# Kernel optimization log

Hardware: AMD Instinct MI355X
Metric: run time of the kernel (lower is better)

Reference implementation:

```python
import jax, jax.numpy as jnp
import numpy as np
import math

B, C, H, W = 8, 512, 32, 32
NUM_HEADS = 8          # channels // num_head_channels = 512 // 64
NUM_GROUPS = 32        # GroupNorm32
EPS = 1e-5


def setup_inputs() -> dict:
    key = jax.random.key(0)
    k1, k2, k3, k4, k5 = jax.random.split(key, 5)
    x = jax.random.normal(k1, (B, C, H, W), dtype=jnp.float32)
    # GroupNorm affine params (torch init: ones/zeros)
    norm_scale = jnp.ones((C,), dtype=jnp.float32)
    norm_bias = jnp.zeros((C,), dtype=jnp.float32)
    # 1x1 Conv1d weights: qkv maps C -> 3C, proj maps C -> C
    qkv_w = jax.random.normal(k2, (3 * C, C), dtype=jnp.float32) * 0.02
    qkv_b = jax.random.normal(k3, (3 * C,), dtype=jnp.float32) * 0.02
    # NOTE: original zero-inits proj_out; we use small random weights so the
    # block computes non-trivial math (same op structure, same FLOPs).
    proj_w = jax.random.normal(k4, (C, C), dtype=jnp.float32) * 0.02
    proj_b = jax.random.normal(k5, (C,), dtype=jnp.float32) * 0.02
    return {"x": x, "norm_scale": norm_scale, "norm_bias": norm_bias,
            "qkv_w": qkv_w, "qkv_b": qkv_b, "proj_w": proj_w, "proj_b": proj_b}


def _attention_block(x, norm_scale, norm_bias, qkv_w, qkv_b, proj_w, proj_b):
    b, c, h, w = x.shape
    t = h * w
    xf = x.reshape(b, c, t)
    # GroupNorm32: fp32 compute, 32 groups, biased variance, eps=1e-5
    g = xf.astype(jnp.float32).reshape(b, NUM_GROUPS, c // NUM_GROUPS, t)
    mean = g.mean(axis=(2, 3), keepdims=True)
    var = g.var(axis=(2, 3), keepdims=True)
    gn = ((g - mean) * jax.lax.rsqrt(var + EPS)).reshape(b, c, t)
    gn = (gn * norm_scale[None, :, None] + norm_bias[None, :, None]).astype(xf.dtype)
    # 1x1 conv == channel matmul: [B,C,T] -> [B,3C,T]
    qkv = jnp.einsum('oc,bct->bot', qkv_w, gn) + qkv_b[None, :, None]
    # Legacy head layout: [B, H*3*ch, T] -> [B*H, 3*ch, T]
    ch = c // NUM_HEADS
    qkv = qkv.reshape(b * NUM_HEADS, 3 * ch, t)
    q, k, v = jnp.split(qkv, 3, axis=1)          # each [B*H, ch, T]
    scale = 1.0 / math.sqrt(math.sqrt(ch))
    weight = jnp.einsum('bct,bcs->bts', q * scale, k * scale)  # [B*H, T, T]
    weight = jax.nn.softmax(weight.astype(jnp.float32), axis=-1).astype(qkv.dtype)
    a = jnp.einsum('bts,bcs->bct', weight, v).reshape(b, c, t)
    out = jnp.einsum('oc,bct->bot', proj_w, a) + proj_b[None, :, None]
    return (xf + out).reshape(b, c, h, w)


def reference(x, norm_scale, norm_bias, qkv_w, qkv_b, proj_w, proj_b):
    return _attention_block(x, norm_scale, norm_bias, qkv_w, qkv_b, proj_w, proj_b)
```

## Files before the change

kernel.cpp:

```cpp
#include <hip/hip_runtime.h>
#include <math.h>

#define B_   8
#define C_   512
#define T_   1024
#define G_   32
#define CPG  16
#define NH   8
#define OC3  1536
#define EPS  1e-5f

#define QSCALE 0.18033688011112042f
#define C_OFF  11.541560327111708f

typedef __bf16 bf16;
typedef __bf16 bf16x4 __attribute__((ext_vector_type(4)));
typedef __bf16 bf16x8 __attribute__((ext_vector_type(8)));
typedef float  f32x4  __attribute__((ext_vector_type(4)));

#define MFMA16(a, b, c) __builtin_amdgcn_mfma_f32_16x16x32_bf16((a), (b), (c), 0, 0, 0)

__device__ __forceinline__ float fexp2(float x) {
#if defined(__has_builtin)
#if __has_builtin(__builtin_amdgcn_exp2f)
    return __builtin_amdgcn_exp2f(x);
#else
    return __expf(x * 0.6931471805599453f);
#endif
#else
    return __expf(x * 0.6931471805599453f);
#endif
}

__global__ __launch_bounds__(256) void cvt_w(const float* __restrict__ w,
                                             bf16* __restrict__ wb)
{
    int i = blockIdx.x * 256 + threadIdx.x;
    float4 v = ((const float4*)w)[i];
    bf16x4 o;
    o[0] = (bf16)v.x; o[1] = (bf16)v.y; o[2] = (bf16)v.z; o[3] = (bf16)v.w;
    *(bf16x4*)(wb + (size_t)i * 4) = o;
}

__global__ __launch_bounds__(256) void gn_kernel(const float* __restrict__ x,
                                                 const float* __restrict__ scale,
                                                 const float* __restrict__ bias,
                                                 bf16* __restrict__ gnT)
{
    const int blk = blockIdx.x;
    const int b = blk >> 5, g = blk & 31;
    const size_t base = (size_t)blk * (CPG * T_);
    const float4* xin = (const float4*)(x + base);
    const int tid = threadIdx.x;

    float s = 0.f, ss = 0.f;
    float4 vals[16];
#pragma unroll
    for (int i = 0; i < 16; ++i) {
        float4 v = xin[tid + i * 256];
        vals[i] = v;
        s  += v.x + v.y + v.z + v.w;
        ss += v.x * v.x + v.y * v.y + v.z * v.z + v.w * v.w;
    }

    __shared__ float rs[256], rss[256];
    rs[tid] = s; rss[tid] = ss;
    __syncthreads();
    for (int off = 128; off > 0; off >>= 1) {
        if (tid < off) { rs[tid] += rs[tid + off]; rss[tid] += rss[tid + off]; }
        __syncthreads();
    }
    const float invN = 1.f / (float)(CPG * T_);
    const float mean = rs[0] * invN;
    const float var  = rss[0] * invN - mean * mean;
    const float inv  = rsqrtf(var + EPS);

    const int c0 = g * CPG;
    float sc[16], bi[16];
#pragma unroll
    for (int i = 0; i < 16; ++i) {
        float s_ = scale[c0 + i] * inv;
        sc[i] = s_;
        bi[i] = bias[c0 + i] - mean * s_;
    }
    bf16* ob = gnT + (size_t)b * (T_ * C_) + c0;
#pragma unroll
    for (int tt = 0; tt < 4; ++tt) {
        bf16x8 lo, hi;
#pragma unroll
        for (int i = 0; i < 8; ++i) {
            float v0 = (tt == 0) ? vals[i].x : (tt == 1) ? vals[i].y
                     : (tt == 2) ? vals[i].z : vals[i].w;
            float v1 = (tt == 0) ? vals[i + 8].x : (tt == 1) ? vals[i + 8].y
                     : (tt == 2) ? vals[i + 8].z : vals[i + 8].w;
            lo[i] = (bf16)(v0 * sc[i] + bi[i]);
            hi[i] = (bf16)(v1 * sc[i + 8] + bi[i + 8]);
        }
        bf16* p = ob + (size_t)(4 * tid + tt) * C_;
        *(bf16x8*)p       = lo;
        *(bf16x8*)(p + 8) = hi;
    }
}

__global__ __launch_bounds__(256) void qkv_gemm(const bf16* __restrict__ gnT,
                                                const bf16* __restrict__ Wb,
                                                const float* __restrict__ qkv_b,
                                                bf16* __restrict__ qkvT)
{
    const int b   = blockIdx.z;
    const int seg = blockIdx.y;
    const int o0  = seg * 64;
    const int t0  = blockIdx.x * 64;
    const int tid = threadIdx.x;
    const int lane = tid & 63;
    const int wv   = tid >> 6;
    const int tg = wv >> 1, og = wv & 1;
    const int lq = lane & 15, lg = lane >> 4;

    __shared__ __align__(16) bf16 Ag[64][72];
    __shared__ __align__(16) bf16 Bg[64][72];

    const bf16* gA = gnT + (size_t)b * (T_ * C_) + (size_t)t0 * C_;
    const bf16* gB = Wb + (size_t)o0 * C_;

    f32x4 acc[2][2];
#pragma unroll
    for (int i = 0; i < 2; ++i)
#pragma unroll
        for (int j = 0; j < 2; ++j) { acc[i][j][0]=0.f; acc[i][j][1]=0.f; acc[i][j][2]=0.f; acc[i][j][3]=0.f; }

    for (int k0 = 0; k0 < C_; k0 += 64) {
#pragma unroll
        for (int it = 0; it < 2; ++it) {
            int c = tid + it * 256;
            int r = c >> 3, cp = c & 7;
            *(bf16x8*)&Ag[r][cp * 8] = *(const bf16x8*)(gA + (size_t)r * C_ + k0 + cp * 8);
            *(bf16x8*)&Bg[r][cp * 8] = *(const bf16x8*)(gB + (size_t)r * C_ + k0 + cp * 8);
        }
        __syncthreads();
        bf16x8 af[2][2], bfr[2][2];
#pragma unroll
        for (int mf = 0; mf < 2; ++mf)
#pragma unroll
            for (int kb = 0; kb < 2; ++kb) {
                af[mf][kb]  = *(const bf16x8*)&Ag[tg * 32 + mf * 16 + lq][kb * 32 + lg * 8];
                bfr[mf][kb] = *(const bf16x8*)&Bg[og * 32 + mf * 16 + lq][kb * 32 + lg * 8];
            }
#pragma unroll
        for (int mf = 0; mf < 2; ++mf)
#pragma unroll
            for (int nf = 0; nf < 2; ++nf) {
                acc[mf][nf] = MFMA16(af[mf][0], bfr[nf][0], acc[mf][nf]);
                acc[mf][nf] = MFMA16(af[mf][1], bfr[nf][1], acc[mf][nf]);
            }
        __syncthreads();
    }

    const int which = seg % 3;
    bf16* outb = qkvT + (size_t)(b * 24 + seg) * (T_ * 64);
    if (which != 2) {
        const float osc = (which == 0) ? QSCALE : 1.0f;
#pragma unroll
        for (int nf = 0; nf < 2; ++nf) {
            int ch = og * 32 + nf * 16 + lq;
            float bias = qkv_b[o0 + ch];
#pragma unroll
            for (int mf = 0; mf < 2; ++mf) {
                int tb = t0 + tg * 32 + mf * 16 + lg * 4;
#pragma unroll
                for (int r = 0; r < 4; ++r)
                    outb[(size_t)(tb + r) * 64 + ch] = (bf16)((acc[mf][nf][r] + bias) * osc);
            }
        }
    } else {
#pragma unroll
        for (int nf = 0; nf < 2; ++nf) {
            int ch = og * 32 + nf * 16 + lq;
            float bias = qkv_b[o0 + ch];
#pragma unroll
            for (int mf = 0; mf < 2; ++mf) {
                int tb = t0 + tg * 32 + mf * 16 + lg * 4;
                bf16x4 pb;
#pragma unroll
                for (int r = 0; r < 4; ++r) pb[r] = (bf16)(acc[mf][nf][r] + bias);
                *(bf16x4*)(outb + (size_t)ch * T_ + tb) = pb;
            }
        }
    }
}

__global__ __launch_bounds__(256) void attn_kernel(const bf16* __restrict__ qkvT,
                                                   bf16* __restrict__ aT)
{
    const int id = blockIdx.x;
    const int bh = id & 63;
    const int tile = id >> 6;
    const int tid = threadIdx.x;
    const int lane = tid & 63;
    const int w  = tid >> 6;
    const int lq = lane & 15;
    const int lg = lane >> 4;
    const int q0 = tile * 128 + w * 32;

    const bf16* qb = qkvT + (size_t)(bh * 3 + 0) * (T_ * 64);
    const bf16* kb = qkvT + (size_t)(bh * 3 + 1) * (T_ * 64);
    const bf16* vb = qkvT + (size_t)(bh * 3 + 2) * (T_ * 64);

    __shared__ __align__(16) bf16 ks[64][72];
    __shared__ __align__(16) bf16 vs[64][72];
    __shared__ __align__(16) bf16 ps[4][32][72];

    bf16x8 qf[2][2];
#pragma unroll
    for (int qg = 0; qg < 2; ++qg)
#pragma unroll
        for (int kh = 0; kh < 2; ++kh)
            qf[qg][kh] = *(const bf16x8*)(qb + (size_t)(q0 + qg * 16 + lq) * 64 + kh * 32 + lg * 8);

    f32x4 oacc[2][4];
#pragma unroll
    for (int qg = 0; qg < 2; ++qg)
#pragma unroll
        for (int og = 0; og < 4; ++og) { oacc[qg][og][0]=0.f; oacc[qg][og][1]=0.f; oacc[qg][og][2]=0.f; oacc[qg][og][3]=0.f; }
    float lloc[2] = {0.f, 0.f};

    const int sr = tid >> 3, scp = tid & 7;
    bf16x8 kreg[2], vreg[2];
#pragma unroll
    for (int it = 0; it < 2; ++it) {
        kreg[it] = *(const bf16x8*)(kb + (size_t)(sr + it * 32) * 64 + scp * 8);
        vreg[it] = *(const bf16x8*)(vb + (size_t)(sr + it * 32) * T_ + scp * 8);
    }

    for (int s0 = 0; s0 < T_; s0 += 64) {
        __syncthreads();
#pragma unroll
        for (int it = 0; it < 2; ++it) {
            *(bf16x8*)&ks[sr + it * 32][scp * 8] = kreg[it];
            *(bf16x8*)&vs[sr + it * 32][scp * 8] = vreg[it];
        }
        __syncthreads();
        if (s0 + 64 < T_) {
            int sn = s0 + 64;
#pragma unroll
            for (int it = 0; it < 2; ++it) {
                kreg[it] = *(const bf16x8*)(kb + (size_t)(sn + sr + it * 32) * 64 + scp * 8);
                vreg[it] = *(const bf16x8*)(vb + (size_t)(sr + it * 32) * T_ + sn + scp * 8);
            }
        }

        f32x4 st[2][4];
        f32x4 cinit; cinit[0] = -C_OFF; cinit[1] = -C_OFF; cinit[2] = -C_OFF; cinit[3] = -C_OFF;
#pragma unroll
        for (int g = 0; g < 4; ++g) {
            bf16x8 kf0 = *(const bf16x8*)&ks[g * 16 + lq][lg * 8];
            bf16x8 kf1 = *(const bf16x8*)&ks[g * 16 + lq][32 + lg * 8];
#pragma unroll
            for (int qg = 0; qg < 2; ++qg) {
                st[qg][g] = MFMA16(kf0, qf[qg][0], cinit);
                st[qg][g] = MFMA16(kf1, qf[qg][1], st[qg][g]);
            }
        }
#pragma unroll
        for (int qg = 0; qg < 2; ++qg) {
            float ll = 0.f;
#pragma unroll
            for (int g = 0; g < 4; ++g) {
                bf16x4 pb;
#pragma unroll
                for (int r = 0; r < 4; ++r) {
                    float p = fexp2(st[qg][g][r]);
                    ll += p;
                    pb[r] = (bf16)p;
                }
                *(bf16x4*)&ps[w][qg * 16 + lq][g * 16 + lg * 4] = pb;
            }
            lloc[qg] += ll;
        }
        bf16x8 pa[2][2];
#pragma unroll
        for (int qg = 0; qg < 2; ++qg)
#pragma unroll
            for (int kh = 0; kh < 2; ++kh)
                pa[qg][kh] = *(const bf16x8*)&ps[w][qg * 16 + lq][kh * 32 + lg * 8];
#pragma unroll
        for (int og = 0; og < 4; ++og) {
            bf16x8 vf0 = *(const bf16x8*)&vs[og * 16 + lq][lg * 8];
            bf16x8 vf1 = *(const bf16x8*)&vs[og * 16 + lq][32 + lg * 8];
#pragma unroll
            for (int qg = 0; qg < 2; ++qg) {
                oacc[qg][og] = MFMA16(pa[qg][0], vf0, oacc[qg][og]);
                oacc[qg][og] = MFMA16(pa[qg][1], vf1, oacc[qg][og]);
            }
        }
    }

    const int b = bh >> 3, h = bh & 7;
#pragma unroll
    for (int qg = 0; qg < 2; ++qg) {
        float l = lloc[qg];
        l += __shfl_xor(l, 16);
        l += __shfl_xor(l, 32);
        float linv = 1.f / l;
        float li[4];
#pragma unroll
        for (int r = 0; r < 4; ++r) li[r] = __shfl(linv, lg * 4 + r);
        bf16* ob = aT + ((size_t)b * T_ + q0 + qg * 16 + lg * 4) * C_ + h * 64 + lq;
#pragma unroll
        for (int og = 0; og < 4; ++og)
#pragma unroll
            for (int r = 0; r < 4; ++r)
                ob[(size_t)r * C_ + og * 16] = (bf16)(oacc[qg][og][r] * li[r]);
    }
}

__global__ __launch_bounds__(256) void proj_gemm(const bf16* __restrict__ aT,
                                                 const bf16* __restrict__ PWb,
                                                 const float* __restrict__ proj_b,
                                                 const float* __restrict__ x,
                                                 float* __restrict__ out)
{
    const int b   = blockIdx.z;
    const int o0  = blockIdx.y * 64;
    const int t0  = blockIdx.x * 64;
    const int tid = threadIdx.x;
    const int lane = tid & 63;
    const int wv   = tid >> 6;
    const int tg = wv >> 1, og = wv & 1;
    const int lq = lane & 15, lg = lane >> 4;

    __shared__ __align__(16) bf16 Ag[64][72];
    __shared__ __align__(16) bf16 Bg[64][72];

    const bf16* gA = aT + (size_t)b * (T_ * C_) + (size_t)t0 * C_;
    const bf16* gB = PWb + (size_t)o0 * C_;

    f32x4 acc[2][2];
#pragma unroll
    for (int i = 0; i < 2; ++i)
#pragma unroll
        for (int j = 0; j < 2; ++j) { acc[i][j][0]=0.f; acc[i][j][1]=0.f; acc[i][j][2]=0.f; acc[i][j][3]=0.f; }

    for (int k0 = 0; k0 < C_; k0 += 64) {
#pragma unroll
        for (int it = 0; it < 2; ++it) {
            int c = tid + it * 256;
            int r = c >> 3, cp = c & 7;
            *(bf16x8*)&Ag[r][cp * 8] = *(const bf16x8*)(gA + (size_t)r * C_ + k0 + cp * 8);
            *(bf16x8*)&Bg[r][cp * 8] = *(const bf16x8*)(gB + (size_t)r * C_ + k0 + cp * 8);
        }
        __syncthreads();
        bf16x8 af[2][2], bfr[2][2];
#pragma unroll
        for (int mf = 0; mf < 2; ++mf)
#pragma unroll
            for (int kb = 0; kb < 2; ++kb) {
                af[mf][kb]  = *(const bf16x8*)&Ag[tg * 32 + mf * 16 + lq][kb * 32 + lg * 8];
                bfr[mf][kb] = *(const bf16x8*)&Bg[og * 32 + mf * 16 + lq][kb * 32 + lg * 8];
            }
#pragma unroll
        for (int mf = 0; mf < 2; ++mf)
#pragma unroll
            for (int nf = 0; nf < 2; ++nf) {
                acc[mf][nf] = MFMA16(af[mf][0], bfr[nf][0], acc[mf][nf]);
                acc[mf][nf] = MFMA16(af[mf][1], bfr[nf][1], acc[mf][nf]);
            }
        __syncthreads();
    }

#pragma unroll
    for (int nf = 0; nf < 2; ++nf) {
        int o = o0 + og * 32 + nf * 16 + lq;
        float bias = proj_b[o];
#pragma unroll
        for (int mf = 0; mf < 2; ++mf) {
            int tb = t0 + tg * 32 + mf * 16 + lg * 4;
            size_t idx = ((size_t)b * C_ + o) * T_ + tb;
            float4 xr = *(const float4*)(x + idx);
            float4 rv;
            rv.x = acc[mf][nf][0] + bias + xr.x;
            rv.y = acc[mf][nf][1] + bias + xr.y;
            rv.z = acc[mf][nf][2] + bias + xr.z;
            rv.w = acc[mf][nf][3] + bias + xr.w;
            *(float4*)(out + idx) = rv;
        }
    }
}

extern "C" void kernel_launch(void* const* d_in, const int* in_sizes, int n_in,
                              void* d_out, int out_size, void* d_ws, size_t ws_size,
                              hipStream_t stream)
{
    (void)in_sizes; (void)n_in; (void)out_size; (void)ws_size;
    const float* x      = (const float*)d_in[0];
    const float* nscale = (const float*)d_in[1];
    const float* nbias  = (const float*)d_in[2];
    const float* qkv_w  = (const float*)d_in[3];
    const float* qkv_b  = (const float*)d_in[4];
    const float* proj_w = (const float*)d_in[5];
    const float* proj_b = (const float*)d_in[6];
    float* out = (float*)d_out;

    char* wsb = (char*)d_ws;
    bf16*  gnT  = (bf16*) (wsb);
    bf16*  Wb   = (bf16*) (wsb + (size_t)(8  << 20));
    bf16*  PWb  = Wb + (size_t)OC3 * C_;
    bf16*  qkvT = (bf16*) (wsb + (size_t)(12 << 20));
    bf16*  aT   = (bf16*) (wsb + (size_t)(36 << 20));

    cvt_w<<<768, 256, 0, stream>>>(qkv_w, Wb);
    cvt_w<<<256, 256, 0, stream>>>(proj_w, PWb);
    gn_kernel<<<B_ * G_, 256, 0, stream>>>(x, nscale, nbias, gnT);
    qkv_gemm<<<dim3(T_ / 64, OC3 / 64, B_), 256, 0, stream>>>(gnT, Wb, qkv_b, qkvT);
    attn_kernel<<<512, 256, 0, stream>>>(qkvT, aT);
    proj_gemm<<<dim3(T_ / 64, C_ / 64, B_), 256, 0, stream>>>(aT, PWb, proj_b, x, out);
}
```

Before: 86.92 us.

## Merge QKV and proj GEMMs into 128x128-tile kernel with register prefetch

```diff
diff --git a/kernel.cpp b/kernel.cpp
--- a/kernel.cpp
+++ b/kernel.cpp
@@ -102,88 +102,122 @@
     }
 }
 
-__global__ __launch_bounds__(256) void qkv_gemm(const bf16* __restrict__ gnT,
-                                                const bf16* __restrict__ Wb,
-                                                const float* __restrict__ qkv_b,
-                                                bf16* __restrict__ qkvT)
+template <int MODE>
+__global__ __launch_bounds__(256) void mm128(const bf16* __restrict__ Arows,
+                                             const bf16* __restrict__ Wt,
+                                             const float* __restrict__ bias,
+                                             const float* __restrict__ x,
+                                             void* __restrict__ outp)
 {
     const int b   = blockIdx.z;
-    const int seg = blockIdx.y;
-    const int o0  = seg * 64;
-    const int t0  = blockIdx.x * 64;
+    const int o0  = blockIdx.y * 128;
+    const int t0  = blockIdx.x * 128;
     const int tid = threadIdx.x;
     const int lane = tid & 63;
-    const int wv   = tid >> 6;
-    const int tg = wv >> 1, og = wv & 1;
+    const int w  = tid >> 6;
+    const int wr = w >> 1, wc = w & 1;
     const int lq = lane & 15, lg = lane >> 4;
 
-    __shared__ __align__(16) bf16 Ag[64][72];
-    __shared__ __align__(16) bf16 Bg[64][72];
-
-    const bf16* gA = gnT + (size_t)b * (T_ * C_) + (size_t)t0 * C_;
-    const bf16* gB = Wb + (size_t)o0 * C_;
-
-    f32x4 acc[2][2];
-#pragma unroll
-    for (int i = 0; i < 2; ++i)
-#pragma unroll
-        for (int j = 0; j < 2; ++j) { acc[i][j][0]=0.f; acc[i][j][1]=0.f; acc[i][j][2]=0.f; acc[i][j][3]=0.f; }
+    __shared__ __align__(16) bf16 Ag[128][72];
+    __shared__ __align__(16) bf16 Bg[128][72];
+
+    const bf16* gA = Arows + (size_t)b * (T_ * C_) + (size_t)t0 * C_;
+    const bf16* gB = Wt + (size_t)o0 * C_;
+
+    f32x4 acc[4][4];
+#pragma unroll
+    for (int i = 0; i < 4; ++i)
+#pragma unroll
+        for (int j = 0; j < 4; ++j) { acc[i][j][0]=0.f; acc[i][j][1]=0.f; acc[i][j][2]=0.f; acc[i][j][3]=0.f; }
+
+    bf16x8 areg[4], breg[4];
+#pragma unroll
+    for (int it = 0; it < 4; ++it) {
+        int chunk = it * 256 + tid, row = chunk >> 3, cp = chunk & 7;
+        areg[it] = *(const bf16x8*)(gA + (size_t)row * C_ + cp * 8);
+        breg[it] = *(const bf16x8*)(gB + (size_t)row * C_ + cp * 8);
+    }
 
     for (int k0 = 0; k0 < C_; k0 += 64) {
-#pragma unroll
-        for (int it = 0; it < 2; ++it) {
-            int c = tid + it * 256;
-            int r = c >> 3, cp = c & 7;
-            *(bf16x8*)&Ag[r][cp * 8] = *(const bf16x8*)(gA + (size_t)r * C_ + k0 + cp * 8);
-            *(bf16x8*)&Bg[r][cp * 8] = *(const bf16x8*)(gB + (size_t)r * C_ + k0 + cp * 8);
-        }
-        __syncthreads();
-        bf16x8 af[2][2], bfr[2][2];
-#pragma unroll
-        for (int mf = 0; mf < 2; ++mf)
-#pragma unroll
-            for (int kb = 0; kb < 2; ++kb) {
-                af[mf][kb]  = *(const bf16x8*)&Ag[tg * 32 + mf * 16 + lq][kb * 32 + lg * 8];
-                bfr[mf][kb] = *(const bf16x8*)&Bg[og * 32 + mf * 16 + lq][kb * 32 + lg * 8];
-            }
-#pragma unroll
-        for (int mf = 0; mf < 2; ++mf)
-#pragma unroll
-            for (int nf = 0; nf < 2; ++nf) {
-                acc[mf][nf] = MFMA16(af[mf][0], bfr[nf][0], acc[mf][nf]);
-                acc[mf][nf] = MFMA16(af[mf][1], bfr[nf][1], acc[mf][nf]);
-            }
-        __syncthreads();
-    }
-
-    const int which = seg % 3;
-    bf16* outb = qkvT + (size_t)(b * 24 + seg) * (T_ * 64);
-    if (which != 2) {
-        const float osc = (which == 0) ? QSCALE : 1.0f;
-#pragma unroll
-        for (int nf = 0; nf < 2; ++nf) {
-            int ch = og * 32 + nf * 16 + lq;
-            float bias = qkv_b[o0 + ch];
-#pragma unroll
-            for (int mf = 0; mf < 2; ++mf) {
-                int tb = t0 + tg * 32 + mf * 16 + lg * 4;
-#pragma unroll
-                for (int r = 0; r < 4; ++r)
-                    outb[(size_t)(tb + r) * 64 + ch] = (bf16)((acc[mf][nf][r] + bias) * osc);
+        __syncthreads();
+#pragma unroll
+        for (int it = 0; it < 4; ++it) {
+            int chunk = it * 256 + tid, row = chunk >> 3, cp = chunk & 7;
+            *(bf16x8*)&Ag[row][cp * 8] = areg[it];
+            *(bf16x8*)&Bg[row][cp * 8] = breg[it];
+        }
+        __syncthreads();
+        if (k0 + 64 < C_) {
+#pragma unroll
+            for (int it = 0; it < 4; ++it) {
+                int chunk = it * 256 + tid, row = chunk >> 3, cp = chunk & 7;
+                areg[it] = *(const bf16x8*)(gA + (size_t)row * C_ + k0 + 64 + cp * 8);
+                breg[it] = *(const bf16x8*)(gB + (size_t)row * C_ + k0 + 64 + cp * 8);
+            }
+        }
+#pragma unroll
+        for (int kb = 0; kb < 2; ++kb) {
+            bf16x8 af[4], bfr[4];
+#pragma unroll
+            for (int i = 0; i < 4; ++i) {
+                af[i]  = *(const bf16x8*)&Ag[wr * 64 + i * 16 + lq][kb * 32 + lg * 8];
+                bfr[i] = *(const bf16x8*)&Bg[wc * 64 + i * 16 + lq][kb * 32 + lg * 8];
+            }
+#pragma unroll
+            for (int mf = 0; mf < 4; ++mf)
+#pragma unroll
+                for (int nf = 0; nf < 4; ++nf)
+                    acc[mf][nf] = MFMA16(af[mf], bfr[nf], acc[mf][nf]);
+        }
+    }
+
+    if (MODE == 0) {
+        bf16* qkvT = (bf16*)outp;
+#pragma unroll
+        for (int nf = 0; nf < 4; ++nf) {
+            int chg = o0 + wc * 64 + nf * 16 + lq;
+            int seg = chg >> 6;
+            int which = seg % 3;
+            int chs = chg & 63;
+            float bv = bias[chg];
+            bf16* outb = qkvT + (size_t)(b * 24 + seg) * (T_ * 64);
+            if (which != 2) {
+                float osc = (which == 0) ? QSCALE : 1.0f;
+#pragma unroll
+                for (int mf = 0; mf < 4; ++mf) {
+                    int tb = t0 + wr * 64 + mf * 16 + lg * 4;
+#pragma unroll
+                    for (int r = 0; r < 4; ++r)
+                        outb[(size_t)(tb + r) * 64 + chs] = (bf16)((acc[mf][nf][r] + bv) * osc);
+                }
+            } else {
+#pragma unroll
+                for (int mf = 0; mf < 4; ++mf) {
+                    int tb = t0 + wr * 64 + mf * 16 + lg * 4;
+                    bf16x4 pb;
+#pragma unroll
+                    for (int r = 0; r < 4; ++r) pb[r] = (bf16)(acc[mf][nf][r] + bv);
+                    *(bf16x4*)(outb + (size_t)chs * T_ + tb) = pb;
+                }
             }
         }
     } else {
-#pragma unroll
-        for (int nf = 0; nf < 2; ++nf) {
-            int ch = og * 32 + nf * 16 + lq;
-            float bias = qkv_b[o0 + ch];
-#pragma unroll
-            for (int mf = 0; mf < 2; ++mf) {
-                int tb = t0 + tg * 32 + mf * 16 + lg * 4;
-                bf16x4 pb;
-#pragma unroll
-                for (int r = 0; r < 4; ++r) pb[r] = (bf16)(acc[mf][nf][r] + bias);
-                *(bf16x4*)(outb + (size_t)ch * T_ + tb) = pb;
+        float* out = (float*)outp;
+#pragma unroll
+        for (int nf = 0; nf < 4; ++nf) {
+            int o = o0 + wc * 64 + nf * 16 + lq;
+            float bv = bias[o];
+#pragma unroll
+            for (int mf = 0; mf < 4; ++mf) {
+                int tb = t0 + wr * 64 + mf * 16 + lg * 4;
+                size_t idx = ((size_t)b * C_ + o) * T_ + tb;
+                float4 xr = *(const float4*)(x + idx);
+                float4 rv;
+                rv.x = acc[mf][nf][0] + bv + xr.x;
+                rv.y = acc[mf][nf][1] + bv + xr.y;
+                rv.z = acc[mf][nf][2] + bv + xr.z;
+                rv.w = acc[mf][nf][3] + bv + xr.w;
+                *(float4*)(out + idx) = rv;
             }
         }
     }
@@ -314,79 +348,6 @@
     }
 }
 
-__global__ __launch_bounds__(256) void proj_gemm(const bf16* __restrict__ aT,
-                                                 const bf16* __restrict__ PWb,
-                                                 const float* __restrict__ proj_b,
-                                                 const float* __restrict__ x,
-                                                 float* __restrict__ out)
-{
-    const int b   = blockIdx.z;
-    const int o0  = blockIdx.y * 64;
-    const int t0  = blockIdx.x * 64;
-    const int tid = threadIdx.x;
-    const int lane = tid & 63;
-    const int wv   = tid >> 6;
-    const int tg = wv >> 1, og = wv & 1;
-    const int lq = lane & 15, lg = lane >> 4;
-
-    __shared__ __align__(16) bf16 Ag[64][72];
-    __shared__ __align__(16) bf16 Bg[64][72];
-
-    const bf16* gA = aT + (size_t)b * (T_ * C_) + (size_t)t0 * C_;
-    const bf16* gB = PWb + (size_t)o0 * C_;
-
-    f32x4 acc[2][2];
-#pragma unroll
-    for (int i = 0; i < 2; ++i)
-#pragma unroll
-        for (int j = 0; j < 2; ++j) { acc[i][j][0]=0.f; acc[i][j][1]=0.f; acc[i][j][2]=0.f; acc[i][j][3]=0.f; }
-
-    for (int k0 = 0; k0 < C_; k0 += 64) {
-#pragma unroll
-        for (int it = 0; it < 2; ++it) {
-            int c = tid + it * 256;
-            int r = c >> 3, cp = c & 7;
-            *(bf16x8*)&Ag[r][cp * 8] = *(const bf16x8*)(gA + (size_t)r * C_ + k0 + cp * 8);
-            *(bf16x8*)&Bg[r][cp * 8] = *(const bf16x8*)(gB + (size_t)r * C_ + k0 + cp * 8);
-        }
-        __syncthreads();
-        bf16x8 af[2][2], bfr[2][2];
-#pragma unroll
-        for (int mf = 0; mf < 2; ++mf)
-#pragma unroll
-            for (int kb = 0; kb < 2; ++kb) {
-                af[mf][kb]  = *(const bf16x8*)&Ag[tg * 32 + mf * 16 + lq][kb * 32 + lg * 8];
-                bfr[mf][kb] = *(const bf16x8*)&Bg[og * 32 + mf * 16 + lq][kb * 32 + lg * 8];
-            }
-#pragma unroll
-        for (int mf = 0; mf < 2; ++mf)
-#pragma unroll
-            for (int nf = 0; nf < 2; ++nf) {
-                acc[mf][nf] = MFMA16(af[mf][0], bfr[nf][0], acc[mf][nf]);
-                acc[mf][nf] = MFMA16(af[mf][1], bfr[nf][1], acc[mf][nf]);
-            }
-        __syncthreads();
-    }
-
-#pragma unroll
-    for (int nf = 0; nf < 2; ++nf) {
-        int o = o0 + og * 32 + nf * 16 + lq;
-        float bias = proj_b[o];
-#pragma unroll
-        for (int mf = 0; mf < 2; ++mf) {
-            int tb = t0 + tg * 32 + mf * 16 + lg * 4;
-            size_t idx = ((size_t)b * C_ + o) * T_ + tb;
-            float4 xr = *(const float4*)(x + idx);
-            float4 rv;
-            rv.x = acc[mf][nf][0] + bias + xr.x;
-            rv.y = acc[mf][nf][1] + bias + xr.y;
-            rv.z = acc[mf][nf][2] + bias + xr.z;
-            rv.w = acc[mf][nf][3] + bias + xr.w;
-            *(float4*)(out + idx) = rv;
-        }
-    }
-}
-
 extern "C" void kernel_launch(void* const* d_in, const int* in_sizes, int n_in,
                               void* d_out, int out_size, void* d_ws, size_t ws_size,
                               hipStream_t stream)
@@ -411,7 +372,7 @@
     cvt_w<<<768, 256, 0, stream>>>(qkv_w, Wb);
     cvt_w<<<256, 256, 0, stream>>>(proj_w, PWb);
     gn_kernel<<<B_ * G_, 256, 0, stream>>>(x, nscale, nbias, gnT);
-    qkv_gemm<<<dim3(T_ / 64, OC3 / 64, B_), 256, 0, stream>>>(gnT, Wb, qkv_b, qkvT);
+    mm128<0><<<dim3(T_ / 128, OC3 / 128, B_), 256, 0, stream>>>(gnT, Wb, qkv_b, nullptr, qkvT);
     attn_kernel<<<512, 256, 0, stream>>>(qkvT, aT);
-    proj_gemm<<<dim3(T_ / 64, C_ / 64, B_), 256, 0, stream>>>(aT, PWb, proj_b, x, out);
-}
+    mm128<1><<<dim3(T_ / 128, C_ / 128, B_), 256, 0, stream>>>(aT, PWb, proj_b, x, out);
+}
```

After: 83.06 us. 1.05x faster.
